# Performance work log

Measured on AMD Instinct MI355X. Metric: run time of the kernel, lower is better.

## Reference

```python
import jax, jax.numpy as jnp
import numpy as np

NUM_HEADS = 16
D_MODEL = 1024
D_K = D_MODEL // NUM_HEADS


def setup_inputs() -> dict:
    key = jax.random.key(0)
    ks = jax.random.split(key, 11)
    B, S = 2, 2048
    s = 1.0 / np.sqrt(D_MODEL)
    return {
        "Q": jax.random.normal(ks[0], (B, S, D_MODEL), jnp.float32),
        "K": jax.random.normal(ks[1], (B, S, D_MODEL), jnp.float32),
        "V": jax.random.normal(ks[2], (B, S, D_MODEL), jnp.float32),
        "Wq": jax.random.normal(ks[3], (D_MODEL, D_MODEL), jnp.float32) * s,
        "bq": jnp.zeros((D_MODEL,), jnp.float32),
        "Wk": jax.random.normal(ks[4], (D_MODEL, D_MODEL), jnp.float32) * s,
        "bk": jnp.zeros((D_MODEL,), jnp.float32),
        "Wv": jax.random.normal(ks[5], (D_MODEL, D_MODEL), jnp.float32) * s,
        "bv": jnp.zeros((D_MODEL,), jnp.float32),
        "Wo": jax.random.normal(ks[6], (D_MODEL, D_MODEL), jnp.float32) * s,
        "bo": jnp.zeros((D_MODEL,), jnp.float32),
    }


def _split_heads(x):
    B, S, _ = x.shape
    return x.reshape(B, S, NUM_HEADS, D_K).transpose(0, 2, 1, 3)  # (B,H,S,Dk)


def reference(Q, K, V, Wq, bq, Wk, bk, Wv, bv, Wo, bo):
    q = _split_heads(Q @ Wq + bq)
    k = _split_heads(K @ Wk + bk)
    v = _split_heads(V @ Wv + bv)
    scores = jnp.einsum("bhqd,bhkd->bhqk", q, k) / jnp.sqrt(jnp.asarray(D_K, q.dtype))
    attn = jax.nn.softmax(scores, axis=-1)
    out = jnp.einsum("bhqk,bhkd->bhqd", attn, v)  # (B,H,S,Dk)
    B, H, S, Dk = out.shape
    combined = out.transpose(0, 2, 1, 3).reshape(B, S, H * Dk)
    return combined @ Wo + bo
```

## Files before the change

kernel.cpp:

```cpp
#include <hip/hip_runtime.h>
#include <stdint.h>

#define DM   1024
#define NH   16
#define DKH  64
#define SEQ  2048
#define NB   2

typedef __attribute__((ext_vector_type(8))) short  frag8;
typedef __attribute__((ext_vector_type(4))) short  frag4;
typedef __attribute__((ext_vector_type(4))) short  short4v;
typedef __attribute__((ext_vector_type(8))) short  short8v;
typedef __attribute__((ext_vector_type(4))) float  f32x4;

__device__ __forceinline__ unsigned short f2bf(float x){
  unsigned u = __float_as_uint(x);
  u += 0x7fffu + ((u >> 16) & 1u);
  return (unsigned short)(u >> 16);
}

__device__ __forceinline__ float dev_exp2(float x){
  return __builtin_amdgcn_exp2f(x);
}

#define GLOAD16(GP, LP) __builtin_amdgcn_global_load_lds( \
    (__attribute__((address_space(1))) void*)(GP), \
    (__attribute__((address_space(3))) void*)(LP), 16, 0, 0)

#define LDSFENCE() do{ asm volatile("" ::: "memory"); \
                       __builtin_amdgcn_sched_barrier(0); }while(0)



__global__ __launch_bounds__(256) void cast_qkv(const float* __restrict__ Q,
                                                const float* __restrict__ K,
                                                const float* __restrict__ V,
                                                short* __restrict__ dst){
  const int z = blockIdx.z;
  const float* src = (z == 0) ? Q : (z == 1 ? K : V);
  const int i = (blockIdx.x * 256 + threadIdx.x) * 4;
  float4 f = *(const float4*)(src + i);
  short4v s;
  s.x = (short)f2bf(f.x); s.y = (short)f2bf(f.y);
  s.z = (short)f2bf(f.z); s.w = (short)f2bf(f.w);
  *(short4v*)(dst + (long)z * (SEQ*NB*DM) + i) = s;
}

__global__ __launch_bounds__(256) void wtrans(const float* __restrict__ Wq,
                                              const float* __restrict__ Wk,
                                              const float* __restrict__ Wv,
                                              const float* __restrict__ Wo,
                                              short* __restrict__ wt){
  const int z = blockIdx.z;
  const float* W = (z == 0) ? Wq : (z == 1 ? Wk : (z == 2 ? Wv : Wo));
  short* out = wt + (long)z * (DM*DM);
  __shared__ float t[32][33];
  const int n0 = blockIdx.x * 32, k0 = blockIdx.y * 32;
  const int c = threadIdx.x & 31, r0 = threadIdx.x >> 5;
#pragma unroll
  for (int i = 0; i < 4; ++i){
    int r = r0 + i * 8;
    t[r][c] = W[(k0 + r) * DM + n0 + c];
  }
  __syncthreads();
#pragma unroll
  for (int i = 0; i < 4; ++i){
    int r = r0 + i * 8;
    out[(n0 + r) * DM + k0 + c] = (short)f2bf(t[c][r]);
  }
}

__device__ __forceinline__ void store_out(short* p, float v){ *p = (short)f2bf(v); }
__device__ __forceinline__ void store_out(float* p, float v){ *p = v; }

template<typename OT>
__global__ __launch_bounds__(256) void gemm_bt(const short* __restrict__ Abase, long Astride,
                                               const short* __restrict__ Btbase, long Btstride,
                                               const float* __restrict__ bias0,
                                               const float* __restrict__ bias1,
                                               const float* __restrict__ bias2,
                                               OT* __restrict__ Cbase, long Cstride,
                                               float qscale){
  const int z = blockIdx.z;
  const short* A  = Abase + (long)z * Astride;
  const short* Bt = Btbase + (long)z * Btstride;
  OT* C = Cbase + (long)z * Cstride;
  const float* bias = (z == 0) ? bias0 : (z == 1 ? bias1 : bias2);
  const float scale = (z == 0) ? qscale : 1.0f;
  const int KD = DM, ND = DM;

  __shared__ __align__(16) short As[2][128 * 64];
  __shared__ __align__(16) short Bs[2][128 * 64];

  const int tid = threadIdx.x;
  const int w = tid >> 6, lane = tid & 63, l15 = lane & 15, quad = lane >> 4;
  const int wy = w >> 1, wx = w & 1;
  const int bm = blockIdx.x * 128, bn = blockIdx.y * 128;
  const int lrow = lane >> 3;
  const int lcolsw = (((lane & 7) ^ lrow) & 7) * 8;

  f32x4 acc[4][4] = {};

#define GSTAGE(KT, BSEL) do{                                                    \
  _Pragma("unroll")                                                             \
  for (int i_ = 0; i_ < 4; ++i_){                                               \
    int j_ = w * 4 + i_;                                                        \
    GLOAD16(A  + (bm + j_ * 8 + lrow) * KD + (KT) * 64 + lcolsw,                \
            &As[BSEL][j_ * 512]);                                               \
    GLOAD16(Bt + (bn + j_ * 8 + lrow) * KD + (KT) * 64 + lcolsw,                \
            &Bs[BSEL][j_ * 512]);                                               \
  } }while(0)

#define GCOMPUTE(BS) do{                                                        \
  _Pragma("unroll") for (int ks = 0; ks < 2; ++ks){                             \
    frag8 af[4], bf_[4];                                                        \
    _Pragma("unroll") for (int mt = 0; mt < 4; ++mt)                            \
      af[mt] = *(const frag8*)&As[BS][(wy * 64 + mt * 16 + l15) * 64 +          \
                                      (((ks * 4 + quad) ^ (l15 & 7)) * 8)];     \
    _Pragma("unroll") for (int nt = 0; nt < 4; ++nt)                            \
      bf_[nt] = *(const frag8*)&Bs[BS][(wx * 64 + nt * 16 + l15) * 64 +         \
                                       (((ks * 4 + quad) ^ (l15 & 7)) * 8)];    \
    _Pragma("unroll") for (int mt = 0; mt < 4; ++mt)                            \
      _Pragma("unroll") for (int nt = 0; nt < 4; ++nt)                          \
        acc[mt][nt] = __builtin_amdgcn_mfma_f32_16x16x32_bf16(                  \
            af[mt], bf_[nt], acc[mt][nt], 0, 0, 0);                             \
  } }while(0)

  GSTAGE(0, 0);
  for (int t = 0; t < KD / 64 - 1; ++t){
    GSTAGE(t + 1, (t + 1) & 1);
    asm volatile("s_waitcnt vmcnt(8)" ::: "memory");
    __builtin_amdgcn_s_barrier();
    LDSFENCE();
    GCOMPUTE(t & 1);
    asm volatile("s_waitcnt lgkmcnt(0)" ::: "memory");
    __builtin_amdgcn_sched_barrier(0);
    __builtin_amdgcn_s_barrier();
  }
  asm volatile("s_waitcnt vmcnt(0)" ::: "memory");
  __builtin_amdgcn_s_barrier();
  LDSFENCE();
  GCOMPUTE(1);

#undef GSTAGE
#undef GCOMPUTE

#pragma unroll
  for (int mt = 0; mt < 4; ++mt){
#pragma unroll
    for (int r = 0; r < 4; ++r){
      int m = bm + wy * 64 + mt * 16 + quad * 4 + r;
#pragma unroll
      for (int nt = 0; nt < 4; ++nt){
        int n = bn + wx * 64 + nt * 16 + l15;
        float v = (acc[mt][nt][r] + bias[n]) * scale;
        store_out(&C[(long)m * ND + n], v);
      }
    }
  }
}

template<typename OT>
__global__ __launch_bounds__(256) void gemm64_bt(const short* __restrict__ A,
                                                 const short* __restrict__ Bt,
                                                 const float* __restrict__ bias,
                                                 OT* __restrict__ C,
                                                 float scale){
  const int KD = DM, ND = DM;
  __shared__ __align__(16) short As[2][64 * 64];
  __shared__ __align__(16) short Bs[2][128 * 64];
  const int tid = threadIdx.x;
  const int w = tid >> 6, lane = tid & 63, l15 = lane & 15, quad = lane >> 4;
  const int wy = w >> 1, wx = w & 1;
  const int bm = blockIdx.x * 64, bn = blockIdx.y * 128;
  const int lrow = lane >> 3;
  const int lcolsw = (((lane & 7) ^ lrow) & 7) * 8;
  f32x4 acc[2][4] = {};

#define GSTAGE64(KT, BSEL) do{                                                  \
  _Pragma("unroll")                                                             \
  for (int i_ = 0; i_ < 2; ++i_){                                               \
    int j_ = w * 2 + i_;                                                        \
    GLOAD16(A + (bm + j_ * 8 + lrow) * KD + (KT) * 64 + lcolsw,                 \
            &As[BSEL][j_ * 512]);                                               \
  }                                                                             \
  _Pragma("unroll")                                                             \
  for (int i_ = 0; i_ < 4; ++i_){                                               \
    int j_ = w * 4 + i_;                                                        \
    GLOAD16(Bt + (bn + j_ * 8 + lrow) * KD + (KT) * 64 + lcolsw,                \
            &Bs[BSEL][j_ * 512]);                                               \
  } }while(0)

#define GCOMPUTE64(BS) do{                                                      \
  _Pragma("unroll") for (int ks = 0; ks < 2; ++ks){                             \
    frag8 af[2], bf_[4];                                                        \
    _Pragma("unroll") for (int mt = 0; mt < 2; ++mt)                            \
      af[mt] = *(const frag8*)&As[BS][(wy * 32 + mt * 16 + l15) * 64 +          \
                                      (((ks * 4 + quad) ^ (l15 & 7)) * 8)];     \
    _Pragma("unroll") for (int nt = 0; nt < 4; ++nt)                            \
      bf_[nt] = *(const frag8*)&Bs[BS][(wx * 64 + nt * 16 + l15) * 64 +         \
                                       (((ks * 4 + quad) ^ (l15 & 7)) * 8)];    \
    _Pragma("unroll") for (int mt = 0; mt < 2; ++mt)                            \
      _Pragma("unroll") for (int nt = 0; nt < 4; ++nt)                          \
        acc[mt][nt] = __builtin_amdgcn_mfma_f32_16x16x32_bf16(                  \
            af[mt], bf_[nt], acc[mt][nt], 0, 0, 0);                             \
  } }while(0)

  GSTAGE64(0, 0);
  for (int t = 0; t < KD / 64 - 1; ++t){
    GSTAGE64(t + 1, (t + 1) & 1);
    asm volatile("s_waitcnt vmcnt(6)" ::: "memory");
    __builtin_amdgcn_s_barrier();
    LDSFENCE();
    GCOMPUTE64(t & 1);
    asm volatile("s_waitcnt lgkmcnt(0)" ::: "memory");
    __builtin_amdgcn_sched_barrier(0);
    __builtin_amdgcn_s_barrier();
  }
  asm volatile("s_waitcnt vmcnt(0)" ::: "memory");
  __builtin_amdgcn_s_barrier();
  LDSFENCE();
  GCOMPUTE64(1);

#undef GSTAGE64
#undef GCOMPUTE64

#pragma unroll
  for (int mt = 0; mt < 2; ++mt){
#pragma unroll
    for (int r = 0; r < 4; ++r){
      int m = bm + wy * 32 + mt * 16 + quad * 4 + r;
#pragma unroll
      for (int nt = 0; nt < 4; ++nt){
        int n = bn + wx * 64 + nt * 16 + l15;
        store_out(&C[(long)m * ND + n], (acc[mt][nt][r] + bias[n]) * scale);
      }
    }
  }
}

__global__ __launch_bounds__(256) void vtrans(const short* __restrict__ v,
                                              short* __restrict__ vt){
  const int bh = blockIdx.y;
  const int b = bh >> 4, h = bh & 15;
  const int s0 = blockIdx.x * 64;
  __shared__ short tT[64][66];
  const short* vb = v + ((long)(b * SEQ + s0)) * DM + h * DKH;
  for (int j = threadIdx.x; j < 512; j += 256){
    int row = j >> 3, off = (j & 7) * 8;
    short8v d = *(const short8v*)(vb + row * DM + off);
#pragma unroll
    for (int e = 0; e < 8; ++e) tT[off + e][row] = d[e];
  }
  __syncthreads();
  short* out = vt + (long)bh * (DKH * SEQ) + s0;
  for (int j = threadIdx.x; j < 512; j += 256){
    int dr = j >> 3, soff = (j & 7) * 8;
    short8v o;
#pragma unroll
    for (int e = 0; e < 8; ++e) o[e] = tT[dr][soff + e];
    *(short8v*)(out + dr * SEQ + soff) = o;
  }
}

__global__ __launch_bounds__(256) void flash(const short* __restrict__ q,
                                             const short* __restrict__ k,
                                             const short* __restrict__ vt,
                                             short* __restrict__ comb){
  const int bh = blockIdx.y;
  const int b = bh >> 4, h = bh & 15;
  const int q0 = blockIdx.x * 128;
  const int tid = threadIdx.x;
  const int w = tid >> 6, lane = tid & 63, l15 = lane & 15, quad = lane >> 4;

  __shared__ __align__(16) short Ks[3][64 * 64];
  __shared__ __align__(16) short Vs[3][64 * 64];

  frag8 aq[2][2];
  const short* qb = q + ((long)(b * SEQ + q0 + w * 32)) * DM + h * DKH;
#pragma unroll
  for (int mt = 0; mt < 2; ++mt)
#pragma unroll
    for (int ks = 0; ks < 2; ++ks)
      aq[mt][ks] = *(const frag8*)(qb + (mt * 16 + l15) * DM + ks * 32 + quad * 8);

  frag8 ones8;
#pragma unroll
  for (int e = 0; e < 8; ++e) ones8[e] = (short)0x3F80;

  f32x4 O[2][4] = {};
  f32x4 Lacc[2] = {{0.f,0.f,0.f,0.f},{0.f,0.f,0.f,0.f}};

  const short* kb  = k + ((long)b * SEQ) * DM + h * DKH;
  const short* vtb = vt + (long)bh * (DKH * SEQ);
  const int lrow8 = lane >> 3;
  const int lcolsw = (((lane & 7) ^ lrow8) & 7) * 8;

#define STAGE(KT, BSEL) do{                                                     \
  _Pragma("unroll")                                                             \
  for (int i_ = 0; i_ < 2; ++i_){                                               \
    int jj_ = w * 2 + i_;                                                       \
    int kr_ = 32 * (jj_ >> 2) + 8 * ((jj_ * 2 + (lrow8 >> 2)) & 3)              \
            + 4 * ((jj_ >> 1) & 1) + (lrow8 & 3);                               \
    GLOAD16(kb  + ((KT) * 64 + kr_) * DM + lcolsw,        &Ks[BSEL][jj_ * 512]);\
    GLOAD16(vtb + (jj_ * 8 + lrow8) * SEQ + (KT) * 64 + lcolsw,                 \
            &Vs[BSEL][jj_ * 512]);                                              \
  } }while(0)

#define COMPUTE(BS) do{                                                         \
  __builtin_amdgcn_s_setprio(1);                                                \
  f32x4 scT[2][4];                                                              \
  _Pragma("unroll") for (int mt = 0; mt < 2; ++mt)                              \
    _Pragma("unroll") for (int nt = 0; nt < 4; ++nt)                            \
      scT[mt][nt] = (f32x4){0.f, 0.f, 0.f, 0.f};                                \
  _Pragma("unroll") for (int ks = 0; ks < 2; ++ks){                             \
    _Pragma("unroll") for (int nt = 0; nt < 4; ++nt){                           \
      frag8 ak = *(const frag8*)&Ks[BS][(nt * 16 + l15) * 64 +                  \
                                        (((ks * 4 + quad) ^ (l15 & 7)) * 8)];   \
      _Pragma("unroll") for (int mt = 0; mt < 2; ++mt)                          \
        scT[mt][nt] = __builtin_amdgcn_mfma_f32_16x16x32_bf16(                  \
            ak, aq[mt][ks], scT[mt][nt], 0, 0, 0);                              \
    }                                                                           \
  }                                                                             \
  frag8 ap8[2][2];                                                              \
  _Pragma("unroll") for (int mt = 0; mt < 2; ++mt)                              \
    _Pragma("unroll") for (int c2 = 0; c2 < 2; ++c2){                           \
      frag8 p8;                                                                 \
      _Pragma("unroll") for (int hf = 0; hf < 2; ++hf)                          \
        _Pragma("unroll") for (int r = 0; r < 4; ++r){                          \
          float e = dev_exp2(scT[mt][2 * c2 + hf][r]);                          \
          p8[hf * 4 + r] = (short)((__float_as_uint(e) + 0x8000u) >> 16);       \
        }                                                                       \
      ap8[mt][c2] = p8;                                                         \
    }                                                                           \
  _Pragma("unroll") for (int c2 = 0; c2 < 2; ++c2){                             \
    _Pragma("unroll") for (int dt = 0; dt < 4; ++dt){                           \
      frag8 bv8 = *(const frag8*)&Vs[BS][(dt * 16 + l15) * 64 +                 \
                                         (((c2 * 4 + quad) ^ (l15 & 7)) * 8)];  \
      _Pragma("unroll") for (int mt = 0; mt < 2; ++mt)                          \
        O[mt][dt] = __builtin_amdgcn_mfma_f32_16x16x32_bf16(                    \
            ap8[mt][c2], bv8, O[mt][dt], 0, 0, 0);                              \
    }                                                                           \
    _Pragma("unroll") for (int mt = 0; mt < 2; ++mt)                            \
      Lacc[mt] = __builtin_amdgcn_mfma_f32_16x16x32_bf16(                       \
          ap8[mt][c2], ones8, Lacc[mt], 0, 0, 0);                               \
  }                                                                             \
  __builtin_amdgcn_s_setprio(0);                                                \
}while(0)

#define ITER(KT, BC, BSNEXT) do{                                                \
  STAGE((KT) + 2, BSNEXT);                                                      \
  asm volatile("s_waitcnt vmcnt(8)" ::: "memory");                              \
  __builtin_amdgcn_s_barrier();                                                 \
  LDSFENCE();                                                                   \
  COMPUTE(BC);                                                                  \
  asm volatile("s_waitcnt lgkmcnt(0)" ::: "memory");                            \
  __builtin_amdgcn_sched_barrier(0);                                            \
  __builtin_amdgcn_s_barrier();                                                 \
}while(0)

  STAGE(0, 0);
  STAGE(1, 1);
  for (int kt = 0; kt < SEQ / 64 - 2; kt += 3){
    ITER(kt,     0, 2);
    ITER(kt + 1, 1, 0);
    ITER(kt + 2, 2, 1);
  }
  asm volatile("s_waitcnt vmcnt(4)" ::: "memory");
  __builtin_amdgcn_s_barrier();
  LDSFENCE();
  COMPUTE(0);
  asm volatile("s_waitcnt vmcnt(0)" ::: "memory");
  __builtin_amdgcn_s_barrier();
  LDSFENCE();
  COMPUTE(1);

#undef ITER
#undef COMPUTE
#undef STAGE

  short* ob = comb + ((long)(b * SEQ + q0 + w * 32)) * DM + h * DKH;
#pragma unroll
  for (int mt = 0; mt < 2; ++mt){
#pragma unroll
    for (int r = 0; r < 4; ++r){
      float inv = 1.f / Lacc[mt][r];
#pragma unroll
      for (int dt = 0; dt < 4; ++dt)
        ob[(mt * 16 + quad * 4 + r) * DM + dt * 16 + l15] = (short)f2bf(O[mt][dt][r] * inv);
    }
  }
}

extern "C" void kernel_launch(void* const* d_in, const int* in_sizes, int n_in,
                              void* d_out, int out_size, void* d_ws, size_t ws_size,
                              hipStream_t stream){
  const float* Q  = (const float*)d_in[0];
  const float* K  = (const float*)d_in[1];
  const float* V  = (const float*)d_in[2];
  const float* Wq = (const float*)d_in[3];
  const float* bq = (const float*)d_in[4];
  const float* Wk = (const float*)d_in[5];
  const float* bk = (const float*)d_in[6];
  const float* Wv = (const float*)d_in[7];
  const float* bv = (const float*)d_in[8];
  const float* Wo = (const float*)d_in[9];
  const float* bo = (const float*)d_in[10];
  float* out = (float*)d_out;

  const long TEN = (long)NB * SEQ * DM;
  const long WEL = (long)DM * DM;
  short* ws   = (short*)d_ws;
  short* xc   = ws;
  short* wt   = xc + 3 * TEN;
  short* qkv  = wt + 4 * WEL;
  short* vtr  = qkv + 3 * TEN;
  short* comb = vtr + TEN;

  cast_qkv<<<dim3(4096, 1, 3), 256, 0, stream>>>(Q, K, V, xc);
  wtrans<<<dim3(32, 32, 4), 256, 0, stream>>>(Wq, Wk, Wv, Wo, wt);
  gemm_bt<short><<<dim3(32, 8, 3), 256, 0, stream>>>(xc, TEN, wt, WEL, bq, bk, bv,
                                                     qkv, TEN, 0.125f * 1.44269504f);
  vtrans<<<dim3(32, 32), 256, 0, stream>>>(qkv + 2 * TEN, vtr);
  flash<<<dim3(16, 32), 256, 0, stream>>>(qkv, qkv + TEN, vtr, comb);
  gemm64_bt<float><<<dim3(64, 8), 256, 0, stream>>>(comb, wt + 3 * WEL, bo, out, 1.0f);
  (void)in_sizes; (void)n_in; (void)out_size; (void)ws_size;
}
```

Baseline: 224.3 us.

## Halve flash query tile to 64 rows and switch to double-buffered K/V pipeline

```diff
diff --git a/kernel.cpp b/kernel.cpp
--- a/kernel.cpp
+++ b/kernel.cpp
@@ -269,27 +269,25 @@
                                              short* __restrict__ comb){
   const int bh = blockIdx.y;
   const int b = bh >> 4, h = bh & 15;
-  const int q0 = blockIdx.x * 128;
+  const int q0 = blockIdx.x * 64;
   const int tid = threadIdx.x;
   const int w = tid >> 6, lane = tid & 63, l15 = lane & 15, quad = lane >> 4;
 
-  __shared__ __align__(16) short Ks[3][64 * 64];
-  __shared__ __align__(16) short Vs[3][64 * 64];
-
-  frag8 aq[2][2];
-  const short* qb = q + ((long)(b * SEQ + q0 + w * 32)) * DM + h * DKH;
-#pragma unroll
-  for (int mt = 0; mt < 2; ++mt)
-#pragma unroll
-    for (int ks = 0; ks < 2; ++ks)
-      aq[mt][ks] = *(const frag8*)(qb + (mt * 16 + l15) * DM + ks * 32 + quad * 8);
+  __shared__ __align__(16) short Ks[2][64 * 64];
+  __shared__ __align__(16) short Vs[2][64 * 64];
+
+  frag8 aq[2];
+  const short* qb = q + ((long)(b * SEQ + q0 + w * 16)) * DM + h * DKH;
+#pragma unroll
+  for (int ks = 0; ks < 2; ++ks)
+    aq[ks] = *(const frag8*)(qb + l15 * DM + ks * 32 + quad * 8);
 
   frag8 ones8;
 #pragma unroll
   for (int e = 0; e < 8; ++e) ones8[e] = (short)0x3F80;
 
-  f32x4 O[2][4] = {};
-  f32x4 Lacc[2] = {{0.f,0.f,0.f,0.f},{0.f,0.f,0.f,0.f}};
+  f32x4 O[4] = {};
+  f32x4 Lacc = {0.f, 0.f, 0.f, 0.f};
 
   const short* kb  = k + ((long)b * SEQ) * DM + h * DKH;
   const short* vtb = vt + (long)bh * (DKH * SEQ);
@@ -309,86 +307,66 @@
 
 #define COMPUTE(BS) do{                                                         \
   __builtin_amdgcn_s_setprio(1);                                                \
-  f32x4 scT[2][4];                                                              \
-  _Pragma("unroll") for (int mt = 0; mt < 2; ++mt)                              \
-    _Pragma("unroll") for (int nt = 0; nt < 4; ++nt)                            \
-      scT[mt][nt] = (f32x4){0.f, 0.f, 0.f, 0.f};                                \
+  f32x4 scT[4];                                                                 \
+  _Pragma("unroll") for (int nt = 0; nt < 4; ++nt)                              \
+    scT[nt] = (f32x4){0.f, 0.f, 0.f, 0.f};                                      \
   _Pragma("unroll") for (int ks = 0; ks < 2; ++ks){                             \
     _Pragma("unroll") for (int nt = 0; nt < 4; ++nt){                           \
       frag8 ak = *(const frag8*)&Ks[BS][(nt * 16 + l15) * 64 +                  \
                                         (((ks * 4 + quad) ^ (l15 & 7)) * 8)];   \
-      _Pragma("unroll") for (int mt = 0; mt < 2; ++mt)                          \
-        scT[mt][nt] = __builtin_amdgcn_mfma_f32_16x16x32_bf16(                  \
-            ak, aq[mt][ks], scT[mt][nt], 0, 0, 0);                              \
+      scT[nt] = __builtin_amdgcn_mfma_f32_16x16x32_bf16(                        \
+          ak, aq[ks], scT[nt], 0, 0, 0);                                        \
     }                                                                           \
   }                                                                             \
-  frag8 ap8[2][2];                                                              \
-  _Pragma("unroll") for (int mt = 0; mt < 2; ++mt)                              \
-    _Pragma("unroll") for (int c2 = 0; c2 < 2; ++c2){                           \
-      frag8 p8;                                                                 \
-      _Pragma("unroll") for (int hf = 0; hf < 2; ++hf)                          \
-        _Pragma("unroll") for (int r = 0; r < 4; ++r){                          \
-          float e = dev_exp2(scT[mt][2 * c2 + hf][r]);                          \
-          p8[hf * 4 + r] = (short)((__float_as_uint(e) + 0x8000u) >> 16);       \
-        }                                                                       \
-      ap8[mt][c2] = p8;                                                         \
-    }                                                                           \
+  frag8 ap8[2];                                                                 \
+  _Pragma("unroll") for (int c2 = 0; c2 < 2; ++c2){                             \
+    frag8 p8;                                                                   \
+    _Pragma("unroll") for (int hf = 0; hf < 2; ++hf)                            \
+      _Pragma("unroll") for (int r = 0; r < 4; ++r){                            \
+        float e = dev_exp2(scT[2 * c2 + hf][r]);                                \
+        p8[hf * 4 + r] = (short)((__float_as_uint(e) + 0x8000u) >> 16);         \
+      }                                                                         \
+    ap8[c2] = p8;                                                               \
+  }                                                                             \
   _Pragma("unroll") for (int c2 = 0; c2 < 2; ++c2){                             \
     _Pragma("unroll") for (int dt = 0; dt < 4; ++dt){                           \
       frag8 bv8 = *(const frag8*)&Vs[BS][(dt * 16 + l15) * 64 +                 \
                                          (((c2 * 4 + quad) ^ (l15 & 7)) * 8)];  \
-      _Pragma("unroll") for (int mt = 0; mt < 2; ++mt)                          \
-        O[mt][dt] = __builtin_amdgcn_mfma_f32_16x16x32_bf16(                    \
-            ap8[mt][c2], bv8, O[mt][dt], 0, 0, 0);                              \
+      O[dt] = __builtin_amdgcn_mfma_f32_16x16x32_bf16(                          \
+          ap8[c2], bv8, O[dt], 0, 0, 0);                                        \
     }                                                                           \
-    _Pragma("unroll") for (int mt = 0; mt < 2; ++mt)                            \
-      Lacc[mt] = __builtin_amdgcn_mfma_f32_16x16x32_bf16(                       \
-          ap8[mt][c2], ones8, Lacc[mt], 0, 0, 0);                               \
+    Lacc = __builtin_amdgcn_mfma_f32_16x16x32_bf16(                             \
+        ap8[c2], ones8, Lacc, 0, 0, 0);                                         \
   }                                                                             \
   __builtin_amdgcn_s_setprio(0);                                                \
 }while(0)
 
-#define ITER(KT, BC, BSNEXT) do{                                                \
-  STAGE((KT) + 2, BSNEXT);                                                      \
-  asm volatile("s_waitcnt vmcnt(8)" ::: "memory");                              \
-  __builtin_amdgcn_s_barrier();                                                 \
-  LDSFENCE();                                                                   \
-  COMPUTE(BC);                                                                  \
-  asm volatile("s_waitcnt lgkmcnt(0)" ::: "memory");                            \
-  __builtin_amdgcn_sched_barrier(0);                                            \
-  __builtin_amdgcn_s_barrier();                                                 \
-}while(0)
-
   STAGE(0, 0);
-  STAGE(1, 1);
-  for (int kt = 0; kt < SEQ / 64 - 2; kt += 3){
-    ITER(kt,     0, 2);
-    ITER(kt + 1, 1, 0);
-    ITER(kt + 2, 2, 1);
-  }
-  asm volatile("s_waitcnt vmcnt(4)" ::: "memory");
-  __builtin_amdgcn_s_barrier();
-  LDSFENCE();
-  COMPUTE(0);
+  for (int t = 0; t < SEQ / 64 - 1; ++t){
+    STAGE(t + 1, (t + 1) & 1);
+    asm volatile("s_waitcnt vmcnt(4)" ::: "memory");
+    __builtin_amdgcn_s_barrier();
+    LDSFENCE();
+    COMPUTE(t & 1);
+    asm volatile("s_waitcnt lgkmcnt(0)" ::: "memory");
+    __builtin_amdgcn_sched_barrier(0);
+    __builtin_amdgcn_s_barrier();
+  }
   asm volatile("s_waitcnt vmcnt(0)" ::: "memory");
   __builtin_amdgcn_s_barrier();
   LDSFENCE();
   COMPUTE(1);
 
-#undef ITER
 #undef COMPUTE
 #undef STAGE
 
-  short* ob = comb + ((long)(b * SEQ + q0 + w * 32)) * DM + h * DKH;
-#pragma unroll
-  for (int mt = 0; mt < 2; ++mt){
-#pragma unroll
-    for (int r = 0; r < 4; ++r){
-      float inv = 1.f / Lacc[mt][r];
-#pragma unroll
-      for (int dt = 0; dt < 4; ++dt)
-        ob[(mt * 16 + quad * 4 + r) * DM + dt * 16 + l15] = (short)f2bf(O[mt][dt][r] * inv);
-    }
+  short* ob = comb + ((long)(b * SEQ + q0 + w * 16)) * DM + h * DKH;
+#pragma unroll
+  for (int r = 0; r < 4; ++r){
+    float inv = 1.f / Lacc[r];
+#pragma unroll
+    for (int dt = 0; dt < 4; ++dt)
+      ob[(quad * 4 + r) * DM + dt * 16 + l15] = (short)f2bf(O[dt][r] * inv);
   }
 }
 
@@ -422,7 +400,7 @@
   gemm_bt<short><<<dim3(32, 8, 3), 256, 0, stream>>>(xc, TEN, wt, WEL, bq, bk, bv,
                                                      qkv, TEN, 0.125f * 1.44269504f);
   vtrans<<<dim3(32, 32), 256, 0, stream>>>(qkv + 2 * TEN, vtr);
-  flash<<<dim3(16, 32), 256, 0, stream>>>(qkv, qkv + TEN, vtr, comb);
+  flash<<<dim3(32, 32), 256, 0, stream>>>(qkv, qkv + TEN, vtr, comb);
   gemm64_bt<float><<<dim3(64, 8), 256, 0, stream>>>(comb, wt + 3 * WEL, bo, out, 1.0f);
   (void)in_sizes; (void)n_in; (void)out_size; (void)ws_size;
 }
```

Result: slower. 230.6 us (+2.8%).
